# Kernel tuning notes

Hardware: AMD Instinct MI355X
Metric: run time of the kernel (lower is better)

Reference implementation:

```python
import jax, jax.numpy as jnp
import numpy as np

RADIUS = 5
EPS = 1e-08


def _box_blur(x, r):
    """Normalized (2r+1)x(2r+1) box filter with reflect padding, NCHW."""
    k = 2 * r + 1
    B, C, H, W = x.shape
    xp = jnp.pad(x, ((0, 0), (0, 0), (r, r), (r, r)), mode='reflect')
    y = xp.reshape(B * C, 1, H + 2 * r, W + 2 * r)
    kh = jnp.ones((1, 1, k, 1), x.dtype) / k
    kw = jnp.ones((1, 1, 1, k), x.dtype) / k
    y = jax.lax.conv_general_dilated(y, kh, (1, 1), 'VALID')
    y = jax.lax.conv_general_dilated(y, kw, (1, 1), 'VALID')
    return y.reshape(B, C, H, W)


def setup_inputs() -> dict:
    key = jax.random.key(0)
    k1, k2 = jax.random.split(key)
    feat = jax.random.uniform(k1, (8, 16, 512, 512), dtype=jnp.float32)
    img = jax.random.uniform(k2, (8, 1, 512, 512), dtype=jnp.float32)
    return {"feat": feat, "img": img}


def reference(feat, img):
    r, eps = RADIUS, EPS
    # scalar-guidance guided filter (guidance img has 1 channel)
    mean_I = _box_blur(img, r)                  # [B,1,H,W]
    mean_p = _box_blur(feat, r)                 # [B,D,H,W]
    corr_I = _box_blur(img * img, r)            # [B,1,H,W]
    corr_Ip = _box_blur(img * feat, r)          # [B,D,H,W]
    var_I = corr_I - mean_I * mean_I
    cov_Ip = corr_Ip - mean_I * mean_p
    a = cov_Ip / (var_I + eps)                  # [B,D,H,W]
    b = mean_p - a * mean_I                     # [B,D,H,W]
    mean_a = _box_blur(a, r)
    mean_b = _box_blur(b, r)
    return mean_a * img + mean_b
```

## Files before the change

kernel.cpp:

```cpp
#include <hip/hip_runtime.h>

#define HH 512
#define WW 512
#define HW (512*512)
#define NB 8
#define ND 16
#define TW 64
#define TH 64
#define VR 74
#define PTW 172

__device__ __forceinline__ int reflect(int v) {
    if (v < 0) v = -v;
    if (v >= HH) v = 2*HH - 2 - v;
    return v;
}

__global__ __launch_bounds__(256) void img_stats(const float* __restrict__ img,
                                                 float2* __restrict__ miv) {
    const int VRs = 42, PTs = 86, THs = 32, TWs = 64;
    __shared__ __align__(16) float hBuf[2*VRs*PTs + 20];
    float* hF = hBuf;
    float* hP = hBuf + VRs*PTs + 20;

    int blk  = blockIdx.x;
    int tile = blk & 127;
    int b    = blk >> 7;
    int ty0  = (tile >> 3) * THs;
    int tx0  = (tile & 7)  * TWs;

    const float inv121 = 1.0f/121.0f;
    const float* ib = img + (size_t)b*HW;
    const int t = threadIdx.x;

    if (t < 252) {
        int seg = t / 84, col = t - seg*84;
        int gx = reflect(tx0 - 10 + col);
        const float* icol = ib + gx;
        int vr0 = seg*14;
        float rv[11], rq[11];
        float sv = 0.f, sq = 0.f;
        #pragma unroll
        for (int j = 0; j < 10; ++j) {
            int gy = reflect(ty0 - 10 + vr0 + j);
            float v = icol[gy*WW], q = v*v;
            rv[j] = v; rq[j] = q; sv += v; sq += q;
        }
        #pragma unroll
        for (int k = 0; k < 14; ++k) {
            int vr = vr0 + k;
            int gy = reflect(ty0 + vr);
            float v = icol[gy*WW], q = v*v;
            sv += v; sq += q;
            hF[vr*PTs + col] = sv;
            hP[vr*PTs + col] = sq;
            sv -= rv[k%11]; sq -= rq[k%11];
            rv[(k+10)%11] = v; rq[(k+10)%11] = q;
        }
    }
    __syncthreads();

    if (t < 168) {
        int arr = t & 1;
        int j2  = t >> 1;
        int seg = (j2 >= 42) ? 1 : 0;
        int vr  = j2 - seg*42;
        int xb = seg ? 38 : 0;
        int nout = seg ? 18 : 19;
        float* rA = (arr ? hP : hF) + vr*PTs;
        float2 ring[5];
        float T = 0.f;
        #pragma unroll
        for (int j = 0; j < 5; ++j) {
            float2 v = *(float2*)(rA + xb + 2*j);
            ring[j] = v; T += v.x + v.y;
        }
        #pragma unroll
        for (int k2 = 0; k2 < 19; ++k2) {
            if (k2 < nout) {
                int hc = xb + 2*k2;
                float2 p = *(float2*)(rA + hc + 10);
                float2 q = ring[k2 % 5];
                float O0 = T + p.x;
                float O1 = O0 + p.y - q.x;
                T = O1 - q.y;
                ring[k2 % 5] = p;
                float2 o; o.x = O0*inv121; o.y = O1*inv121;
                *(float2*)(rA + hc + 10*seg) = o;
            }
        }
    }
    __syncthreads();

    float2* mb = miv + (size_t)b*HW;
    for (int i = t; i < THs*TWs; i += 256) {
        int y = i >> 6, x = i & 63;
        int vr = y + 5, hc = x + 5;
        int slot = hc + ((hc >= 38) ? 10 : 0);
        float mI  = hF[vr*PTs + slot];
        float mII = hP[vr*PTs + slot];
        float var = mII - mI*mI;
        float2 o; o.x = mI; o.y = 1.0f / (var + 1e-8f);
        mb[(ty0 + y)*WW + tx0 + x] = o;
    }
}

__global__ __launch_bounds__(512) void guided_main(const float* __restrict__ feat,
                                                   const float* __restrict__ img,
                                                   const float2* __restrict__ miv,
                                                   float* __restrict__ out) {
    __shared__ __align__(16) float S[VR*PTW];

    int blk  = blockIdx.x;
    int tile = blk & 63;
    int bd   = blk >> 6;
    int b    = bd >> 4;
    int ty0  = (tile >> 3) * TH;
    int tx0  = (tile & 7)  * TW;

    const float inv121 = 1.0f/121.0f;
    const float* fb   = feat + (size_t)bd*HW;
    const float* ib   = img  + (size_t)b*HW;
    const float2* mivb = miv + (size_t)b*HW;
    const int t = threadIdx.x;

    if (t < 504) {
        int seg = t / 84, col = t - seg*84;
        int gx = reflect(tx0 - 10 + col);
        const float* fcol = fb + gx;
        const float* icol = ib + gx;
        int vr0 = seg*13;
        float rf[11], rp[11];
        float sf = 0.f, sp = 0.f;
        #pragma unroll
        for (int j = 0; j < 10; ++j) {
            int gy = reflect(ty0 - 10 + vr0 + j);
            float f = fcol[gy*WW], im = icol[gy*WW];
            float p = f*im;
            rf[j] = f; rp[j] = p; sf += f; sp += p;
        }
        #pragma unroll
        for (int k = 0; k < 13; ++k) {
            int vr = vr0 + k;
            if (vr < VR) {
                int gy = reflect(ty0 + vr);
                float f = fcol[gy*WW], im = icol[gy*WW];
                float p = f*im;
                sf += f; sp += p;
                float2 st; st.x = sf; st.y = sp;
                *(float2*)(S + vr*PTW + 2*col) = st;
                sf -= rf[k%11]; sp -= rp[k%11];
                rf[(k+10)%11] = f; rp[(k+10)%11] = p;
            }
        }
    }
    __syncthreads();

    if (t < 148) {
        int seg = (t >= 74) ? 1 : 0;
        int vr  = t - seg*74;
        float* row = S + vr*PTW;
        int xbu = seg*19;
        int nout = seg ? 18 : 19;
        float4 ring[5];
        float TF = 0.f, TP = 0.f;
        #pragma unroll
        for (int j = 0; j < 5; ++j) {
            float4 v = *(float4*)(row + 4*(xbu + j));
            ring[j] = v; TF += v.x + v.z; TP += v.y + v.w;
        }
        #pragma unroll
        for (int k = 0; k < 19; ++k) {
            if (k < nout) {
                float4 p = *(float4*)(row + 4*(xbu + 5 + k));
                float4 q = ring[k % 5];
                float O0f = TF + p.x;
                float O1f = O0f + p.z - q.x;
                TF = O1f - q.z;
                float O0p = TP + p.y;
                float O1p = O0p + p.w - q.y;
                TP = O1p - q.w;
                ring[k % 5] = p;
                float4 o;
                o.x = O0f*inv121; o.y = O0p*inv121;
                o.z = O1f*inv121; o.w = O1p*inv121;
                *(float4*)(row + 4*(k + xbu + 5*seg)) = o;
            }
        }
    }
    __syncthreads();

    for (int i = t; i < VR*37; i += 512) {
        int y = i / 37, u = i - y*37;
        int su = u + ((u >= 19) ? 5 : 0);
        float* cell = S + y*PTW + 4*su;
        float4 mc = *(float4*)cell;
        int gy = reflect(ty0 - 5 + y);
        const float2* mrow = mivb + gy*WW;
        int gx0 = tx0 - 5 + 2*u;
        float2 g0 = mrow[reflect(gx0)];
        float2 g1 = mrow[reflect(gx0+1)];
        float a0 = (mc.y - g0.x*mc.x) * g0.y;
        float b0 = mc.x - a0*g0.x;
        float a1 = (mc.w - g1.x*mc.z) * g1.y;
        float b1 = mc.z - a1*g1.x;
        float4 o; o.x = a0; o.y = b0; o.z = a1; o.w = b1;
        *(float4*)cell = o;
    }
    __syncthreads();

    if (t < 148) {
        int seg = (t >= 74) ? 1 : 0;
        int c   = t - seg*74;
        int sw  = 2*(c + ((c >= 38) ? 10 : 0));
        int y0  = seg*32;
        float2 ring[11];
        float sa = 0.f, sb = 0.f;
        #pragma unroll
        for (int j = 0; j < 10; ++j) {
            float2 v = *(float2*)(S + (y0+j)*PTW + sw);
            ring[j] = v; sa += v.x; sb += v.y;
        }
        #pragma unroll
        for (int k = 0; k < 32; ++k) {
            int y = y0 + k;
            float2 v = *(float2*)(S + (y+10)*PTW + sw);
            sa += v.x; sb += v.y;
            int wrow = y + 10*seg;
            float2 o; o.x = sa; o.y = sb;
            *(float2*)(S + wrow*PTW + sw) = o;
            sa -= ring[k%11].x; sb -= ring[k%11].y;
            ring[(k+10)%11] = v;
        }
    }
    __syncthreads();

    if (t < 128) {
        int seg = t >> 6, row = t & 63;
        int prow = row + ((row >= 32) ? 10 : 0);
        float* rw = S + prow*PTW;
        int ub = seg*16;
        float4 ring[5];
        float TA = 0.f, TB = 0.f;
        #pragma unroll
        for (int j = 0; j < 5; ++j) {
            int u = ub + j; int su = u + ((u >= 19) ? 5 : 0);
            float4 v = *(float4*)(rw + 4*su);
            ring[j] = v; TA += v.x + v.z; TB += v.y + v.w;
        }
        #pragma unroll
        for (int k = 0; k < 16; ++k) {
            int u = ub + 5 + k; int su = u + ((u >= 19) ? 5 : 0);
            float4 p = *(float4*)(rw + 4*su);
            float4 q = ring[k % 5];
            float A0 = TA + p.x;
            float A1 = A0 + p.z - q.x;
            TA = A1 - q.z;
            float B0 = TB + p.y;
            float B1 = B0 + p.w - q.y;
            TB = B1 - q.w;
            ring[k % 5] = p;
            float4 o; o.x = A0; o.y = B0; o.z = A1; o.w = B1;
            *(float4*)(rw + 4*(ub + k) + 40*seg) = o;
        }
    }
    __syncthreads();

    float* ob = out + (size_t)bd*HW;
    for (int i = t; i < TH*32; i += 512) {
        int row = i >> 5, u = i & 31;
        int prow = row + ((row >= 32) ? 10 : 0);
        int ww = 4*u + ((u >= 16) ? 40 : 0);
        float4 s4 = *(float4*)(S + prow*PTW + ww);
        int gy = ty0 + row;
        int x0 = 2*u;
        float2 im2 = *(const float2*)(ib + gy*WW + tx0 + x0);
        float2 o;
        o.x = (s4.x*im2.x + s4.y)*inv121;
        o.y = (s4.z*im2.y + s4.w)*inv121;
        *(float2*)(ob + gy*WW + tx0 + x0) = o;
    }
}

extern "C" void kernel_launch(void* const* d_in, const int* in_sizes, int n_in,
                              void* d_out, int out_size, void* d_ws, size_t ws_size,
                              hipStream_t stream) {
    const float* feat = (const float*)d_in[0];
    const float* img  = (const float*)d_in[1];
    float* out  = (float*)d_out;
    float2* miv = (float2*)d_ws;

    img_stats<<<NB*128, 256, 0, stream>>>(img, miv);
    guided_main<<<NB*ND*64, 512, 0, stream>>>(feat, img, miv, out);
}
```

Measured before the change: 153.1 us.

## Restructure guided filter into wavefront-scan tiles with fused a/b computation

Replaces the 64x64 tile pipeline of separate shared-memory passes with 44-wide by 128-tall tiles, one 64-lane wavefront per column strip. The horizontal box sums are now computed in registers with a DPP/shuffle prefix scan, and the a/b coefficients are formed in the same vertical sweep, which removes several shared-memory passes and barriers. The narrower tiles raise the halo overhead (64 columns loaded for 44 outputs), and the last tile overlaps its neighbour to cover the 512-wide edge. The scans also add cross-lane shuffle work for every row.

```diff
diff --git a/kernel.cpp b/kernel.cpp
--- a/kernel.cpp
+++ b/kernel.cpp
@@ -5,15 +5,56 @@
 #define HW (512*512)
 #define NB 8
 #define ND 16
-#define TW 64
-#define TH 64
-#define VR 74
-#define PTW 172
+#define W  44
+#define AW 54
+#define TH 128
+#define AR 138
+#define PAB 110
+#define NX 12
+#define NY 4
 
 __device__ __forceinline__ int reflect(int v) {
     if (v < 0) v = -v;
     if (v >= HH) v = 2*HH - 2 - v;
     return v;
+}
+
+#if defined(__has_builtin)
+#if __has_builtin(__builtin_amdgcn_update_dpp)
+#define HAVE_DPP 1
+#endif
+#endif
+__device__ __forceinline__ float iscan64(float x) {
+#ifdef HAVE_DPP
+    int ti;
+#define DPPSTEP(ctrl, rmask)                                                   \
+    ti = __builtin_amdgcn_update_dpp(0, __builtin_bit_cast(int, x),            \
+                                     ctrl, rmask, 0xf, true);                  \
+    x += __builtin_bit_cast(float, ti);
+    DPPSTEP(0x111, 0xf)
+    DPPSTEP(0x112, 0xf)
+    DPPSTEP(0x114, 0xf)
+    DPPSTEP(0x118, 0xf)
+    DPPSTEP(0x142, 0xa)
+    DPPSTEP(0x143, 0xc)
+#undef DPPSTEP
+    return x;
+#else
+    int l = threadIdx.x & 63;
+    #pragma unroll
+    for (int d = 1; d < 64; d <<= 1) {
+        float t = __shfl_up(x, d);
+        if (l >= d) x += t;
+    }
+    return x;
+#endif
+}
+
+__device__ __forceinline__ float box11(float P, int l) {
+    float hi = __shfl(P, l + 5);
+    int lm = l - 6;
+    float lo = __shfl(P, lm < 0 ? 0 : lm);
+    return hi - (lm < 0 ? 0.f : lo);
 }
 
 __global__ __launch_bounds__(256) void img_stats(const float* __restrict__ img,
@@ -94,7 +135,8 @@
 
     float2* mb = miv + (size_t)b*HW;
     for (int i = t; i < THs*TWs; i += 256) {
-        int y = i >> 6, x = i & 63;
+        int y = i >> 5;
+        y = i >> 6; int x = i & 63;
         int vr = y + 5, hc = x + 5;
         int slot = hc + ((hc >= 38) ? 10 : 0);
         float mI  = hF[vr*PTs + slot];
@@ -109,46 +151,58 @@
                                                    const float* __restrict__ img,
                                                    const float2* __restrict__ miv,
                                                    float* __restrict__ out) {
-    __shared__ __align__(16) float S[VR*PTW];
+    __shared__ __align__(16) float AB[AR*PAB + 4];
 
     int blk  = blockIdx.x;
-    int tile = blk & 63;
-    int bd   = blk >> 6;
+    int bd   = blk / (NX*NY);
+    int tile = blk - bd*(NX*NY);
+    int xt   = tile % NX;
+    int yt   = tile / NX;
+    int x0   = (xt < NX-1) ? W*xt : (WW - W);
+    int ty0  = yt * TH;
     int b    = bd >> 4;
-    int ty0  = (tile >> 3) * TH;
-    int tx0  = (tile & 7)  * TW;
 
     const float inv121 = 1.0f/121.0f;
     const float* fb   = feat + (size_t)bd*HW;
     const float* ib   = img  + (size_t)b*HW;
     const float2* mivb = miv + (size_t)b*HW;
     const int t = threadIdx.x;
-
-    if (t < 504) {
-        int seg = t / 84, col = t - seg*84;
-        int gx = reflect(tx0 - 10 + col);
-        const float* fcol = fb + gx;
-        const float* icol = ib + gx;
-        int vr0 = seg*13;
+    const int wv = t >> 6, l = t & 63;
+
+    {
+        int rgx = reflect(x0 - 10 + l);
+        const float* fcol = fb + rgx;
+        const float* icol = ib + rgx;
+        int rs = (AR * wv) >> 3;
+        int re = (AR * (wv+1)) >> 3;
+        int nout = re - rs;
         float rf[11], rp[11];
         float sf = 0.f, sp = 0.f;
         #pragma unroll
         for (int j = 0; j < 10; ++j) {
-            int gy = reflect(ty0 - 10 + vr0 + j);
-            float f = fcol[gy*WW], im = icol[gy*WW];
-            float p = f*im;
+            int gy = reflect(ty0 + rs - 10 + j);
+            float f = fcol[gy*WW], p = f * icol[gy*WW];
             rf[j] = f; rp[j] = p; sf += f; sp += p;
         }
         #pragma unroll
-        for (int k = 0; k < 13; ++k) {
-            int vr = vr0 + k;
-            if (vr < VR) {
-                int gy = reflect(ty0 + vr);
-                float f = fcol[gy*WW], im = icol[gy*WW];
-                float p = f*im;
+        for (int k = 0; k < 18; ++k) {
+            if (k < nout) {
+                int r = rs + k;
+                int gy = reflect(ty0 + r);
+                float f = fcol[gy*WW], p = f * icol[gy*WW];
                 sf += f; sp += p;
-                float2 st; st.x = sf; st.y = sp;
-                *(float2*)(S + vr*PTW + 2*col) = st;
+                float PF = iscan64(sf);
+                float PP = iscan64(sp);
+                float mp  = box11(PF, l) * inv121;
+                float cip = box11(PP, l) * inv121;
+                int gya = reflect(ty0 + r - 5);
+                float2 g = mivb[gya*WW + rgx];
+                float a  = (cip - g.x*mp) * g.y;
+                float bb = mp - a*g.x;
+                if (l >= 5 && l <= 58) {
+                    float2 o; o.x = a; o.y = bb;
+                    *(float2*)(AB + r*PAB + 2*(l-5)) = o;
+                }
                 sf -= rf[k%11]; sp -= rp[k%11];
                 rf[(k+10)%11] = f; rp[(k+10)%11] = p;
             }
@@ -156,129 +210,36 @@
     }
     __syncthreads();
 
-    if (t < 148) {
-        int seg = (t >= 74) ? 1 : 0;
-        int vr  = t - seg*74;
-        float* row = S + vr*PTW;
-        int xbu = seg*19;
-        int nout = seg ? 18 : 19;
-        float4 ring[5];
-        float TF = 0.f, TP = 0.f;
-        #pragma unroll
-        for (int j = 0; j < 5; ++j) {
-            float4 v = *(float4*)(row + 4*(xbu + j));
-            ring[j] = v; TF += v.x + v.z; TP += v.y + v.w;
-        }
-        #pragma unroll
-        for (int k = 0; k < 19; ++k) {
-            if (k < nout) {
-                float4 p = *(float4*)(row + 4*(xbu + 5 + k));
-                float4 q = ring[k % 5];
-                float O0f = TF + p.x;
-                float O1f = O0f + p.z - q.x;
-                TF = O1f - q.z;
-                float O0p = TP + p.y;
-                float O1p = O0p + p.w - q.y;
-                TP = O1p - q.w;
-                ring[k % 5] = p;
-                float4 o;
-                o.x = O0f*inv121; o.y = O0p*inv121;
-                o.z = O1f*inv121; o.w = O1p*inv121;
-                *(float4*)(row + 4*(k + xbu + 5*seg)) = o;
+    {
+        int cl = (l < AW) ? l : (AW-1);
+        int rix = reflect(x0 - 5 + l);
+        int ys = wv * 16;
+        float2 ra[11];
+        float sa = 0.f, sb = 0.f;
+        #pragma unroll
+        for (int j = 0; j < 10; ++j) {
+            float2 v = *(const float2*)(AB + (ys + j)*PAB + 2*cl);
+            ra[j] = v; sa += v.x; sb += v.y;
+        }
+        float* ob = out + (size_t)bd*HW;
+        #pragma unroll
+        for (int k = 0; k < 16; ++k) {
+            int y = ys + k;
+            float2 v = *(const float2*)(AB + (y + 10)*PAB + 2*cl);
+            sa += v.x; sb += v.y;
+            float PA = iscan64(sa);
+            float PB = iscan64(sb);
+            float suma = box11(PA, l);
+            float sumb = box11(PB, l);
+            int gy = ty0 + y;
+            float im = ib[gy*WW + rix];
+            float o = (suma * im + sumb) * inv121;
+            if (l >= 5 && l <= 48) {
+                ob[gy*WW + (x0 + l - 5)] = o;
             }
-        }
-    }
-    __syncthreads();
-
-    for (int i = t; i < VR*37; i += 512) {
-        int y = i / 37, u = i - y*37;
-        int su = u + ((u >= 19) ? 5 : 0);
-        float* cell = S + y*PTW + 4*su;
-        float4 mc = *(float4*)cell;
-        int gy = reflect(ty0 - 5 + y);
-        const float2* mrow = mivb + gy*WW;
-        int gx0 = tx0 - 5 + 2*u;
-        float2 g0 = mrow[reflect(gx0)];
-        float2 g1 = mrow[reflect(gx0+1)];
-        float a0 = (mc.y - g0.x*mc.x) * g0.y;
-        float b0 = mc.x - a0*g0.x;
-        float a1 = (mc.w - g1.x*mc.z) * g1.y;
-        float b1 = mc.z - a1*g1.x;
-        float4 o; o.x = a0; o.y = b0; o.z = a1; o.w = b1;
-        *(float4*)cell = o;
-    }
-    __syncthreads();
-
-    if (t < 148) {
-        int seg = (t >= 74) ? 1 : 0;
-        int c   = t - seg*74;
-        int sw  = 2*(c + ((c >= 38) ? 10 : 0));
-        int y0  = seg*32;
-        float2 ring[11];
-        float sa = 0.f, sb = 0.f;
-        #pragma unroll
-        for (int j = 0; j < 10; ++j) {
-            float2 v = *(float2*)(S + (y0+j)*PTW + sw);
-            ring[j] = v; sa += v.x; sb += v.y;
-        }
-        #pragma unroll
-        for (int k = 0; k < 32; ++k) {
-            int y = y0 + k;
-            float2 v = *(float2*)(S + (y+10)*PTW + sw);
-            sa += v.x; sb += v.y;
-            int wrow = y + 10*seg;
-            float2 o; o.x = sa; o.y = sb;
-            *(float2*)(S + wrow*PTW + sw) = o;
-            sa -= ring[k%11].x; sb -= ring[k%11].y;
-            ring[(k+10)%11] = v;
-        }
-    }
-    __syncthreads();
-
-    if (t < 128) {
-        int seg = t >> 6, row = t & 63;
-        int prow = row + ((row >= 32) ? 10 : 0);
-        float* rw = S + prow*PTW;
-        int ub = seg*16;
-        float4 ring[5];
-        float TA = 0.f, TB = 0.f;
-        #pragma unroll
-        for (int j = 0; j < 5; ++j) {
-            int u = ub + j; int su = u + ((u >= 19) ? 5 : 0);
-            float4 v = *(float4*)(rw + 4*su);
-            ring[j] = v; TA += v.x + v.z; TB += v.y + v.w;
-        }
-        #pragma unroll
-        for (int k = 0; k < 16; ++k) {
-            int u = ub + 5 + k; int su = u + ((u >= 19) ? 5 : 0);
-            float4 p = *(float4*)(rw + 4*su);
-            float4 q = ring[k % 5];
-            float A0 = TA + p.x;
-            float A1 = A0 + p.z - q.x;
-            TA = A1 - q.z;
-            float B0 = TB + p.y;
-            float B1 = B0 + p.w - q.y;
-            TB = B1 - q.w;
-            ring[k % 5] = p;
-            float4 o; o.x = A0; o.y = B0; o.z = A1; o.w = B1;
-            *(float4*)(rw + 4*(ub + k) + 40*seg) = o;
-        }
-    }
-    __syncthreads();
-
-    float* ob = out + (size_t)bd*HW;
-    for (int i = t; i < TH*32; i += 512) {
-        int row = i >> 5, u = i & 31;
-        int prow = row + ((row >= 32) ? 10 : 0);
-        int ww = 4*u + ((u >= 16) ? 40 : 0);
-        float4 s4 = *(float4*)(S + prow*PTW + ww);
-        int gy = ty0 + row;
-        int x0 = 2*u;
-        float2 im2 = *(const float2*)(ib + gy*WW + tx0 + x0);
-        float2 o;
-        o.x = (s4.x*im2.x + s4.y)*inv121;
-        o.y = (s4.z*im2.y + s4.w)*inv121;
-        *(float2*)(ob + gy*WW + tx0 + x0) = o;
+            sa -= ra[k%11].x; sb -= ra[k%11].y;
+            ra[(k+10)%11] = v;
+        }
     }
 }
 
@@ -291,5 +252,5 @@
     float2* miv = (float2*)d_ws;
 
     img_stats<<<NB*128, 256, 0, stream>>>(img, miv);
-    guided_main<<<NB*ND*64, 512, 0, stream>>>(feat, img, miv, out);
-}
+    guided_main<<<NX*NY*NB*ND, 512, 0, stream>>>(feat, img, miv, out);
+}
```

Measured after the change: 294.7 us. 92.4% more time.
